# Kernel optimization log

Hardware: AMD Instinct MI355X
Metric: run time of the kernel (lower is better)

## Reference

```python
import jax, jax.numpy as jnp
import numpy as np

EPS = 1e-5

def lrelu(x):
    return jnp.where(x > 0, x, 0.2 * x)

def bn(x, g, b, ch_axis=1):
    # BatchNorm in training-mode math (batch statistics), affine
    axes = tuple(i for i in range(x.ndim) if i != ch_axis)
    m = x.mean(axes, keepdims=True)
    v = x.var(axes, keepdims=True)
    shp = [1] * x.ndim; shp[ch_axis] = -1
    return g.reshape(shp) * (x - m) / jnp.sqrt(v + EPS) + b.reshape(shp)

def get_graph_feature(x, idx):
    # x: (B,C,N), idx: (B,N,k) -> edge features (B,2C,N,k) = [neighbor - center, center]
    xt = jnp.transpose(x, (0, 2, 1))                      # (B,N,C)
    nb = jax.vmap(lambda pts, i: pts[i])(xt, idx)         # gather: (B,N,k,C)
    center = jnp.broadcast_to(xt[:, :, None, :], nb.shape)
    edge = jnp.concatenate([nb - center, center], axis=-1)  # (B,N,k,2C)
    return jnp.transpose(edge, (0, 3, 1, 2))              # (B,2C,N,k)

def setup_inputs() -> dict:
    key = jax.random.key(0)
    ks = jax.random.split(key, 12)
    B, N, K = 4, 2048, 20
    def w(k, o, c, s=0.05):
        return jax.random.normal(k, (o, c), jnp.float32) * s
    inp = {}
    inp["x"] = jax.random.normal(ks[0], (B, N, 3), jnp.float32)
    inp["start_neighs"] = jax.random.randint(ks[1], (B, N, K), 0, N)
    dims = [(6, 64), (128, 128), (256, 256), (512, 512)]
    for i, (ci, co) in enumerate(dims):
        inp["w%d" % i] = w(ks[2 + i], co, ci)
        inp["g%d" % i] = jnp.ones((co,), jnp.float32)
        inp["b%d" % i] = jnp.zeros((co,), jnp.float32)
    inp["w4"] = w(ks[6], 1024, 960)
    inp["g4"] = jnp.ones((1024,), jnp.float32); inp["b4"] = jnp.zeros((1024,), jnp.float32)
    inp["lw1"] = w(ks[7], 1024, 2048)
    inp["g6"] = jnp.ones((1024,), jnp.float32); inp["b6"] = jnp.zeros((1024,), jnp.float32)
    inp["lw2"] = w(ks[8], 512, 1024); inp["lb2"] = jnp.zeros((512,), jnp.float32)
    inp["g7"] = jnp.ones((512,), jnp.float32); inp["b7"] = jnp.zeros((512,), jnp.float32)
    inp["lw3"] = w(ks[9], 256, 512); inp["lb3"] = jnp.zeros((256,), jnp.float32)
    return inp

def reference(x, start_neighs,
              w0, g0, b0, w1, g1, b1, w2, g2, b2, w3, g3, b3,
              w4, g4, b4, lw1, g6, b6, lw2, lb2, g7, b7, lw3, lb3):
    # forward_per_point
    xt = jnp.transpose(x, (0, 2, 1))                      # (B,3,N)
    h = get_graph_feature(xt, start_neighs)               # (B,6,N,k)
    outs = []
    for (w, g, b) in ((w0, g0, b0), (w1, g1, b1), (w2, g2, b2), (w3, g3, b3)):
        if outs:  # only_true_neighs=True -> reuse start_neighs
            h = get_graph_feature(outs[-1], start_neighs)
        h = lrelu(bn(jnp.einsum('oc,bcnk->bonk', w, h), g, b))  # 1x1 Conv2d + BN + LeakyReLU
        outs.append(h.max(axis=-1))                       # max over k neighbors -> (B,C,N)
    cat = jnp.concatenate(outs, axis=1)                   # (B,960,N)
    feats = lrelu(bn(jnp.einsum('oc,bcn->bon', w4, cat), g4, b4))  # (B,1024,N)
    # aggregate_all_points (dropout p=0 -> identity)
    z = jnp.concatenate([feats.max(-1), feats.mean(-1)], axis=1)   # (B,2048)
    z = lrelu(bn(z @ lw1.T, g6, b6))
    z = lrelu(bn(z @ lw2.T + lb2, g7, b7))
    z = z @ lw3.T + lb3                                   # (B,256)
    # forward returns (aggregated.squeeze(-1), features_per_point.transpose(1,2)) = (z, (B,1024,N))
    return z, feats
```

## Files before the change

kernel.cpp:

```cpp
#include <hip/hip_runtime.h>
#include <cstddef>
#include <cstdint>

#define EPSBN 1e-5f
constexpr int B_ = 4, N_ = 2048, K_ = 20;

typedef __attribute__((ext_vector_type(8))) _Float16 half8v;
typedef __attribute__((ext_vector_type(4))) float f32x4;
typedef const __attribute__((address_space(1))) unsigned int* gas_t;
typedef __attribute__((address_space(3))) unsigned int* las_t;

__device__ __forceinline__ void swz_batch(int B, int& b, int& local) {
    b = (B & 7) >> 1;
    local = ((B >> 3) << 1) | (B & 1);
}


__device__ __forceinline__ void prep_conv(const float* __restrict__ W, _Float16* __restrict__ W2h,
                                          int O, int C, int i) {
    int o = i / C, c = i - o * C;
    float a = W[o * 2 * C + c];
    float d = W[o * 2 * C + C + c] - a;
    W2h[(size_t)o * C + c] = (_Float16)a;
    W2h[(size_t)(O + o) * C + c] = (_Float16)d;
}

__global__ void k_prep_all(const float* __restrict__ w1, const float* __restrict__ w2,
                           const float* __restrict__ w3, const float* __restrict__ w4,
                           _Float16* __restrict__ W2h1, _Float16* __restrict__ W2h2,
                           _Float16* __restrict__ W2h3, _Float16* __restrict__ w4h) {
    int i = blockIdx.x * 256 + threadIdx.x;
    if (i < 8192) { prep_conv(w1, W2h1, 128, 64, i); return; }
    i -= 8192;
    if (i < 32768) { prep_conv(w2, W2h2, 256, 128, i); return; }
    i -= 32768;
    if (i < 131072) { prep_conv(w3, W2h3, 512, 256, i); return; }
    i -= 131072;
    if (i < 983040) w4h[i] = (_Float16)w4[i];
}

template<bool STATS, int BM>
__global__ __launch_bounds__(256, 3)
void k_gemm(const _Float16* __restrict__ A, int sa,
            const _Float16* __restrict__ Bw, int K,
            _Float16* __restrict__ outp, int so,
            float* __restrict__ psum, float* __restrict__ psq) {
    constexpr int MI = BM / 32;
    __shared__ __align__(16) _Float16 Als[BM * 64];
    __shared__ __align__(16) _Float16 Bls[128 * 64];
    const int tid = threadIdx.x, lane = tid & 63, w = tid >> 6;
    int bsw, lsw;
    swz_batch(blockIdx.x, bsw, lsw);
    constexpr int TPB = 2048 / BM;
    const int m0 = (bsw * TPB + lsw) * BM;
    const int n0 = blockIdx.y * 128;
    const int wr = (w >> 1) * (BM / 2), wc = (w & 1) * 64;

    f32x4 acc[MI][4];
#pragma unroll
    for (int i = 0; i < MI; ++i)
#pragma unroll
        for (int j = 0; j < 4; ++j) acc[i][j] = (f32x4){0.f, 0.f, 0.f, 0.f};

    int srb[4], scb[4];
#pragma unroll
    for (int j = 0; j < 4; ++j) {
        int idx = w * 256 + j * 64 + lane;
        srb[j] = idx >> 3;
        scb[j] = ((idx & 7) ^ (srb[j] & 7)) * 8;
    }
    int sra[MI], sca[MI];
#pragma unroll
    for (int j = 0; j < MI; ++j) {
        int idx = w * (MI * 64) + j * 64 + lane;
        sra[j] = idx >> 3;
        sca[j] = ((idx & 7) ^ (sra[j] & 7)) * 8;
    }
    int aoff[MI][2], boff[4][2];
#pragma unroll
    for (int i = 0; i < MI; ++i) {
        int ra = wr + i * 16 + (lane & 15);
#pragma unroll
        for (int t = 0; t < 2; ++t)
            aoff[i][t] = ra * 64 + ((((lane >> 4) + t * 4) ^ (ra & 7)) * 8);
    }
#pragma unroll
    for (int j = 0; j < 4; ++j) {
        int rb = wc + j * 16 + (lane & 15);
#pragma unroll
        for (int t = 0; t < 2; ++t)
            boff[j][t] = rb * 64 + ((((lane >> 4) + t * 4) ^ (rb & 7)) * 8);
    }

    for (int c0 = 0; c0 < K; c0 += 64) {
#pragma unroll
        for (int j = 0; j < MI; ++j) {
            const _Float16* ga = &A[(size_t)(m0 + sra[j]) * sa + c0 + sca[j]];
            __builtin_amdgcn_global_load_lds((gas_t)(const void*)ga,
                                             (las_t)(void*)&Als[(w * MI * 64 + j * 64) * 8], 16, 0, 0);
        }
#pragma unroll
        for (int j = 0; j < 4; ++j) {
            const _Float16* gb = &Bw[(size_t)(n0 + srb[j]) * K + c0 + scb[j]];
            __builtin_amdgcn_global_load_lds((gas_t)(const void*)gb,
                                             (las_t)(void*)&Bls[(w * 256 + j * 64) * 8], 16, 0, 0);
        }
        __syncthreads();
#pragma unroll
        for (int t = 0; t < 2; ++t) {
            half8v a[MI], b[4];
#pragma unroll
            for (int i = 0; i < MI; ++i) a[i] = *(const half8v*)&Als[aoff[i][t]];
#pragma unroll
            for (int j = 0; j < 4; ++j) b[j] = *(const half8v*)&Bls[boff[j][t]];
#pragma unroll
            for (int i = 0; i < MI; ++i)
#pragma unroll
                for (int j = 0; j < 4; ++j)
                    acc[i][j] = __builtin_amdgcn_mfma_f32_16x16x32_f16(a[i], b[j], acc[i][j], 0, 0, 0);
        }
        __syncthreads();
    }
#pragma unroll
    for (int i = 0; i < MI; ++i)
#pragma unroll
        for (int j = 0; j < 4; ++j)
#pragma unroll
            for (int e = 0; e < 4; ++e) {
                int row = m0 + wr + i * 16 + (lane >> 4) * 4 + e;
                int col = n0 + wc + j * 16 + (lane & 15);
                outp[(size_t)row * so + col] = (_Float16)acc[i][j][e];
            }
    if constexpr (STATS) {
        int slice = blockIdx.x & 63;
#pragma unroll
        for (int j = 0; j < 4; ++j) {
            float s = 0.f, q = 0.f;
#pragma unroll
            for (int i = 0; i < MI; ++i)
#pragma unroll
                for (int e = 0; e < 4; ++e) {
                    float v = acc[i][j][e];
                    s += v; q += v * v;
                }
            s += __shfl_xor(s, 16); s += __shfl_xor(s, 32);
            q += __shfl_xor(q, 16); q += __shfl_xor(q, 32);
            if ((lane >> 4) == 0) {
                int col = n0 + wc + j * 16 + lane;
                atomicAdd(&psum[slice * 1024 + col], s);
                atomicAdd(&psq[slice * 1024 + col], q);
            }
        }
    }
}

__global__ __launch_bounds__(256)
void k_gather0(const float* __restrict__ x, const float* __restrict__ w0,
               const int* __restrict__ nidx, const float* __restrict__ g,
               _Float16* __restrict__ exth,
               float* __restrict__ psum, float* __restrict__ psq) {
    constexpr int O = 64, VPT = 8, P = 32;
    __shared__ float s_red[P * O];
    __shared__ float q_red[P * O];
    const int tid = threadIdx.x;
    const int pl = tid / VPT, v = tid % VPT;
    int bsw, local;
    swz_batch(blockIdx.x, bsw, local);
    const int bbase = bsw * N_;
    const int p = bbase + local * P + pl;
    float wa[8][3], wd[8][3], sg[8];
#pragma unroll
    for (int e = 0; e < 8; ++e) {
        int o = v * 8 + e;
        float a0 = w0[o * 6], a1 = w0[o * 6 + 1], a2 = w0[o * 6 + 2];
        wa[e][0] = a0; wa[e][1] = a1; wa[e][2] = a2;
        wd[e][0] = w0[o * 6 + 3] - a0;
        wd[e][1] = w0[o * 6 + 4] - a1;
        wd[e][2] = w0[o * 6 + 5] - a2;
        sg[e] = (g[o] >= 0.f) ? 1.f : -1.f;
    }
    float mx[8], sm[8], sq[8];
#pragma unroll
    for (int e = 0; e < 8; ++e) { mx[e] = -3.4e38f; sm[e] = 0.f; sq[e] = 0.f; }
    const int* np = nidx + p * K_;
#pragma unroll 4
    for (int k = 0; k < K_; ++k) {
        int j = bbase + np[k];
        float x0 = x[j * 3], x1 = x[j * 3 + 1], x2 = x[j * 3 + 2];
#pragma unroll
        for (int e = 0; e < 8; ++e) {
            float f = wa[e][0] * x0 + wa[e][1] * x1 + wa[e][2] * x2;
            mx[e] = fmaxf(mx[e], f * sg[e]);
            sm[e] += f;
            sq[e] += f * f;
        }
    }
    float xp0 = x[p * 3], xp1 = x[p * 3 + 1], xp2 = x[p * 3 + 2];
    const float Kf = (float)K_;
    half8v exo;
#pragma unroll
    for (int e = 0; e < 8; ++e) {
        float zf = wd[e][0] * xp0 + wd[e][1] * xp1 + wd[e][2] * xp2;
        exo[e] = (_Float16)(sg[e] * mx[e] + zf);
        s_red[pl * O + v * 8 + e] = sm[e] + Kf * zf;
        q_red[pl * O + v * 8 + e] = sq[e] + 2.f * zf * sm[e] + Kf * zf * zf;
    }
    *(half8v*)&exth[(size_t)p * O + v * 8] = exo;
    __syncthreads();
    int slice = blockIdx.x & 63;
    for (int ch = tid; ch < O; ch += 256) {
        float s = 0.f, q = 0.f;
#pragma unroll
        for (int pp = 0; pp < P; ++pp) { s += s_red[pp * O + ch]; q += q_red[pp * O + ch]; }
        atomicAdd(&psum[slice * 1024 + ch], s);
        atomicAdd(&psq[slice * 1024 + ch], q);
    }
}

template<int O>
__global__ __launch_bounds__(256)
void k_gather(const _Float16* __restrict__ Z, const int* __restrict__ nidx,
              const float* __restrict__ g,
              _Float16* __restrict__ exth,
              float* __restrict__ psum, float* __restrict__ psq) {
    constexpr int VPT = O / 8, P = 256 / VPT;
    __shared__ float s_red[P * O];
    __shared__ float q_red[P * O];
    const int tid = threadIdx.x;
    const int pl = tid / VPT, v = tid % VPT;
    int bsw, local;
    swz_batch(blockIdx.x, bsw, local);
    const int bbase = bsw * N_;
    const int p = bbase + local * P + pl;
    float sg[8];
#pragma unroll
    for (int e = 0; e < 8; ++e) sg[e] = (g[v * 8 + e] >= 0.f) ? 1.f : -1.f;
    float mx[8], sm[8], sq[8];
#pragma unroll
    for (int e = 0; e < 8; ++e) { mx[e] = -3.4e38f; sm[e] = 0.f; sq[e] = 0.f; }
    const int* np = nidx + p * K_;
#pragma unroll 4
    for (int k = 0; k < K_; ++k) {
        int j = np[k];
        half8v z = *(const half8v*)&Z[(size_t)(bbase + j) * (2 * O) + v * 8];
#pragma unroll
        for (int e = 0; e < 8; ++e) {
            float f = (float)z[e];
            mx[e] = fmaxf(mx[e], f * sg[e]);
            sm[e] += f;
            sq[e] += f * f;
        }
    }
    half8v zd = *(const half8v*)&Z[(size_t)p * (2 * O) + O + v * 8];
    const float Kf = (float)K_;
    half8v exo;
#pragma unroll
    for (int e = 0; e < 8; ++e) {
        float zf = (float)zd[e];
        exo[e] = (_Float16)(sg[e] * mx[e] + zf);
        s_red[pl * O + v * 8 + e] = sm[e] + Kf * zf;
        q_red[pl * O + v * 8 + e] = sq[e] + 2.f * zf * sm[e] + Kf * zf * zf;
    }
    *(half8v*)&exth[(size_t)p * O + v * 8] = exo;
    __syncthreads();
    int slice = blockIdx.x & 63;
    for (int ch = tid; ch < O; ch += 256) {
        float s = 0.f, q = 0.f;
#pragma unroll
        for (int pp = 0; pp < P; ++pp) { s += s_red[pp * O + ch]; q += q_red[pp * O + ch]; }
        atomicAdd(&psum[slice * 1024 + ch], s);
        atomicAdd(&psq[slice * 1024 + ch], q);
    }
}

__global__ void k_finalize_sl(const float* __restrict__ psum, const float* __restrict__ psq,
                              const float* __restrict__ g, const float* __restrict__ b,
                              float cntInv, int O,
                              float* __restrict__ scale, float* __restrict__ shift) {
    int o = blockIdx.x * 256 + threadIdx.x;
    if (o >= O) return;
    float s = 0.f, q = 0.f;
    for (int i = 0; i < 64; ++i) { s += psum[i * 1024 + o]; q += psq[i * 1024 + o]; }
    float m = s * cntInv;
    float v = q * cntInv - m * m;
    float sc = g[o] * rsqrtf(fmaxf(v, 0.f) + EPSBN);
    scale[o] = sc;
    shift[o] = b[o] - m * sc;
}

template<int O>
__global__ void k_bn_apply(const _Float16* __restrict__ exth,
                           const float* __restrict__ scale, const float* __restrict__ shift,
                           _Float16* __restrict__ cath, int coff) {
    constexpr int PPB = 2048 / O;
    int bsw, local;
    swz_batch(blockIdx.x, bsw, local);
    const int pt_base = bsw * N_ + local * PPB;
    int tid = threadIdx.x;
    int pt = pt_base + (tid * 8) / O;
    int v8 = (tid * 8) & (O - 1);
    half8v hx = *(const half8v*)&exth[(size_t)pt * O + v8];
    half8v r;
#pragma unroll
    for (int e = 0; e < 8; ++e) {
        int o = v8 + e;
        float y = scale[o] * (float)hx[e] + shift[o];
        y = y > 0.f ? y : 0.2f * y;
        r[e] = (_Float16)y;
    }
    *(half8v*)&cath[(size_t)pt * 960 + coff + v8] = r;
}

__global__ void k_feats_out(const _Float16* __restrict__ Y4, const float* __restrict__ scale,
                            const float* __restrict__ shift, float* __restrict__ fo,
                            float* __restrict__ pmax, float* __restrict__ psumn) {
    __shared__ float tile[32][33];
    int tx = threadIdx.x, ty = threadIdx.y;
    int b = blockIdx.z;
    int n0 = blockIdx.x * 32, c0 = blockIdx.y * 32;
#pragma unroll
    for (int i = 0; i < 4; ++i) {
        int n = n0 + ty + i * 8;
        int c = c0 + tx;
        float v = (float)Y4[((size_t)(b * N_ + n)) * 1024 + c];
        v = scale[c] * v + shift[c];
        v = v > 0.f ? v : 0.2f * v;
        tile[ty + i * 8][tx] = v;
    }
    __syncthreads();
#pragma unroll
    for (int i = 0; i < 4; ++i) {
        int c = c0 + ty + i * 8;
        int n = n0 + tx;
        float v2 = tile[tx][ty + i * 8];
        fo[((size_t)(b * 1024 + c)) * N_ + n] = v2;
        float mx = v2, s = v2;
#pragma unroll
        for (int d = 1; d < 32; d <<= 1) {
            mx = fmaxf(mx, __shfl_xor(mx, d));
            s += __shfl_xor(s, d);
        }
        if (tx == 0) {
            int bc = (b << 10) + c;
            pmax[(size_t)bc * 64 + blockIdx.x] = mx;
            psumn[(size_t)bc * 64 + blockIdx.x] = s;
        }
    }
}

__global__ void k_pool2(const float* __restrict__ pmax, const float* __restrict__ psumn,
                        float* __restrict__ z0) {
    int bc = blockIdx.x * 4 + (threadIdx.x >> 6);
    int lane = threadIdx.x & 63;
    float mx = pmax[(size_t)bc * 64 + lane];
    float s  = psumn[(size_t)bc * 64 + lane];
#pragma unroll
    for (int d = 1; d < 64; d <<= 1) {
        mx = fmaxf(mx, __shfl_xor(mx, d));
        s += __shfl_xor(s, d);
    }
    if (lane == 0) {
        int b = bc >> 10, c = bc & 1023;
        z0[b * 2048 + c] = mx;
        z0[b * 2048 + 1024 + c] = s * (1.f / N_);
    }
}

__global__ void k_fc(const float* __restrict__ zin, const float* __restrict__ W,
                     const float* __restrict__ bias,
                     const float* __restrict__ gg, const float* __restrict__ gb,
                     int C, int O, float* __restrict__ zout) {
    __shared__ float sh4[4];
    const int b = threadIdx.x >> 6;
    const int lane = threadIdx.x & 63;
    const int o = blockIdx.x;
    const float* wr = W + (size_t)o * C;
    const float* zr = zin + b * C;
    float s = 0.f;
    for (int c = lane * 4; c < C; c += 256) {
        const float4 wv = *(const float4*)&wr[c];
        const float4 zv = *(const float4*)&zr[c];
        s += wv.x * zv.x + wv.y * zv.y + wv.z * zv.z + wv.w * zv.w;
    }
    s += __shfl_xor(s, 1);
    s += __shfl_xor(s, 2);
    s += __shfl_xor(s, 4);
    s += __shfl_xor(s, 8);
    s += __shfl_xor(s, 16);
    s += __shfl_xor(s, 32);
    if (!gg) {
        if (lane == 0) zout[b * O + o] = s + (bias ? bias[o] : 0.f);
        return;
    }
    if (lane == 0) sh4[b] = s + (bias ? bias[o] : 0.f);
    __syncthreads();
    if (threadIdx.x == 0) {
        float v0 = sh4[0], v1 = sh4[1], v2 = sh4[2], v3 = sh4[3];
        float m = 0.25f * (v0 + v1 + v2 + v3);
        float d0 = v0 - m, d1 = v1 - m, d2 = v2 - m, d3 = v3 - m;
        float var = 0.25f * (d0 * d0 + d1 * d1 + d2 * d2 + d3 * d3);
        float sc = gg[o] * rsqrtf(var + EPSBN);
        float shv = gb[o];
        float r0 = sc * d0 + shv, r1 = sc * d1 + shv, r2 = sc * d2 + shv, r3 = sc * d3 + shv;
        zout[o]         = r0 > 0.f ? r0 : 0.2f * r0;
        zout[O + o]     = r1 > 0.f ? r1 : 0.2f * r1;
        zout[2 * O + o] = r2 > 0.f ? r2 : 0.2f * r2;
        zout[3 * O + o] = r3 > 0.f ? r3 : 0.2f * r3;
    }
}


extern "C" void kernel_launch(void* const* d_in, const int* in_sizes, int n_in,
                              void* d_out, int out_size, void* d_ws, size_t ws_size,
                              hipStream_t stream) {
    const float* x    = (const float*)d_in[0];
    const int*   nidx = (const int*)d_in[1];
    const float* w[5]  = {(const float*)d_in[2], (const float*)d_in[5], (const float*)d_in[8],
                          (const float*)d_in[11], (const float*)d_in[14]};
    const float* g[5]  = {(const float*)d_in[3], (const float*)d_in[6], (const float*)d_in[9],
                          (const float*)d_in[12], (const float*)d_in[15]};
    const float* bb[5] = {(const float*)d_in[4], (const float*)d_in[7], (const float*)d_in[10],
                          (const float*)d_in[13], (const float*)d_in[16]};
    const float* lw1 = (const float*)d_in[17];
    const float* g6  = (const float*)d_in[18];
    const float* b6  = (const float*)d_in[19];
    const float* lw2 = (const float*)d_in[20];
    const float* lb2 = (const float*)d_in[21];
    const float* g7  = (const float*)d_in[22];
    const float* b7  = (const float*)d_in[23];
    const float* lw3 = (const float*)d_in[24];
    const float* lb3 = (const float*)d_in[25];

    float* out = (float*)d_out;
    float* fo  = out + 1024;

    uint8_t* base8 = (uint8_t*)d_ws;
    size_t off = 0;
    auto alloc = [&](size_t bytes) -> void* {
        void* r = base8 + off;
        off += (bytes + 255) & ~(size_t)255;
        return r;
    };
    _Float16* cath = (_Float16*)alloc((size_t)B_ * N_ * 960 * 2);
    _Float16* Z    = (_Float16*)alloc((size_t)8192 * 1024 * 2);
    _Float16* exth = (_Float16*)alloc((size_t)8192 * 512 * 2);
    _Float16* Y4   = (_Float16*)alloc((size_t)8192 * 1024 * 2);
    _Float16* W2h1 = (_Float16*)alloc((size_t)256 * 64 * 2);
    _Float16* W2h2 = (_Float16*)alloc((size_t)512 * 128 * 2);
    _Float16* W2h3 = (_Float16*)alloc((size_t)1024 * 256 * 2);
    _Float16* w4h  = (_Float16*)alloc((size_t)1024 * 960 * 2);
    float* psumall = (float*)alloc((size_t)5 * 131072 * 4);
    float* pmax  = (float*)alloc((size_t)4096 * 64 * 4);
    float* psumn = (float*)alloc((size_t)4096 * 64 * 4);
    float* scalev= (float*)alloc(1024 * 4);
    float* shiftv= (float*)alloc(1024 * 4);
    float* z0    = (float*)alloc(8192 * 4);
    float* z1    = (float*)alloc(4096 * 4);
    float* z2    = (float*)alloc(2048 * 4);
    (void)ws_size; (void)in_sizes; (void)n_in; (void)out_size;

    auto psumR = [&](int r) { return psumall + (size_t)r * 131072; };
    auto psqR  = [&](int r) { return psumall + (size_t)r * 131072 + 65536; };

    hipMemsetAsync(psumall, 0, (size_t)5 * 131072 * 4, stream);
    k_prep_all<<<(8192 + 32768 + 131072 + 983040 + 255) / 256, 256, 0, stream>>>(
        w[1], w[2], w[3], w[4], W2h1, W2h2, W2h3, w4h);

    k_gather0<<<256, 256, 0, stream>>>(x, w[0], nidx, g[0], exth, psumR(0), psqR(0));
    k_finalize_sl<<<1, 256, 0, stream>>>(psumR(0), psqR(0), g[0], bb[0], 1.f / (B_ * N_ * K_),
                                         64, scalev, shiftv);
    k_bn_apply<64><<<256, 256, 0, stream>>>(exth, scalev, shiftv, cath, 0);

    k_gemm<false, 64><<<dim3(128, 2), 256, 0, stream>>>(cath + 0, 960, W2h1, 64,
                                                        Z, 256, nullptr, nullptr);
    k_gather<128><<<512, 256, 0, stream>>>(Z, nidx, g[1], exth, psumR(1), psqR(1));
    k_finalize_sl<<<1, 256, 0, stream>>>(psumR(1), psqR(1), g[1], bb[1],
                                         1.f / (B_ * N_ * K_), 128, scalev, shiftv);
    k_bn_apply<128><<<512, 256, 0, stream>>>(exth, scalev, shiftv, cath, 64);

    k_gemm<false, 128><<<dim3(64, 4), 256, 0, stream>>>(cath + 64, 960, W2h2, 128,
                                                        Z, 512, nullptr, nullptr);
    k_gather<256><<<1024, 256, 0, stream>>>(Z, nidx, g[2], exth, psumR(2), psqR(2));
    k_finalize_sl<<<1, 256, 0, stream>>>(psumR(2), psqR(2), g[2], bb[2],
                                         1.f / (B_ * N_ * K_), 256, scalev, shiftv);
    k_bn_apply<256><<<1024, 256, 0, stream>>>(exth, scalev, shiftv, cath, 192);

    k_gemm<false, 128><<<dim3(64, 8), 256, 0, stream>>>(cath + 192, 960, W2h3, 256,
                                                        Z, 1024, nullptr, nullptr);
    k_gather<512><<<2048, 256, 0, stream>>>(Z, nidx, g[3], exth, psumR(3), psqR(3));
    k_finalize_sl<<<2, 256, 0, stream>>>(psumR(3), psqR(3), g[3], bb[3],
                                         1.f / (B_ * N_ * K_), 512, scalev, shiftv);
    k_bn_apply<512><<<2048, 256, 0, stream>>>(exth, scalev, shiftv, cath, 448);

    k_gemm<true, 128><<<dim3(64, 8), 256, 0, stream>>>(cath, 960, w4h, 960, Y4, 1024,
                                                       psumR(4), psqR(4));
    k_finalize_sl<<<4, 256, 0, stream>>>(psumR(4), psqR(4), g[4], bb[4], 1.f / (B_ * N_), 1024,
                                         scalev, shiftv);
    k_feats_out<<<dim3(64, 32, 4), dim3(32, 8), 0, stream>>>(Y4, scalev, shiftv, fo, pmax, psumn);
    k_pool2<<<1024, 256, 0, stream>>>(pmax, psumn, z0);

    k_fc<<<1024, 256, 0, stream>>>(z0, lw1, nullptr, g6, b6, 2048, 1024, z1);
    k_fc<<<512, 256, 0, stream>>>(z1, lw2, lb2, g7, b7, 1024, 512, z2);
    k_fc<<<256, 256, 0, stream>>>(z2, lw3, lb3, nullptr, nullptr, 512, 256, out);
}
```

Baseline: 168.9 us.

## Fuse BN finalize into apply kernels and pool via atomics into FC input

Replaces each per-layer finalize+apply kernel pair with one kernel that reduces the per-slice sums for its 64-channel tile and then applies BN+LeakyReLU. The global max/mean pooling kernel is removed: the feats kernel does an atomic max on an order-preserving uint key and an atomic add on the sum into z0, which is zeroed by an extended memset. The first FC decodes the keys and scales the mean. This cuts five kernel launches, but each BN block now redundantly rereads the 64-slice partial sums, and the pooling adds atomic contention.

```diff
diff --git a/kernel.cpp b/kernel.cpp
--- a/kernel.cpp
+++ b/kernel.cpp
@@ -13,6 +13,15 @@
 __device__ __forceinline__ void swz_batch(int B, int& b, int& local) {
     b = (B & 7) >> 1;
     local = ((B >> 3) << 1) | (B & 1);
+}
+
+__device__ __forceinline__ unsigned fkey(float x) {
+    unsigned u = __float_as_uint(x);
+    return (u & 0x80000000u) ? ~u : (u | 0x80000000u);
+}
+__device__ __forceinline__ float funkey(unsigned k) {
+    unsigned u = (k & 0x80000000u) ? (k ^ 0x80000000u) : ~k;
+    return __uint_as_float(u);
 }
 
 
@@ -273,6 +282,62 @@
     }
 }
 
+template<int O>
+__global__ __launch_bounds__(256)
+void k_bnfin(const _Float16* __restrict__ exth,
+             const float* __restrict__ psum, const float* __restrict__ psq,
+             const float* __restrict__ g, const float* __restrict__ b, float cntInv,
+             _Float16* __restrict__ cath, int coff) {
+    constexpr int NCT = O / 64;
+    __shared__ float part_s[64][4];
+    __shared__ float part_q[64][4];
+    __shared__ float scale_s[64], shift_s[64];
+    const int tid = threadIdx.x;
+    const int ct = blockIdx.x % NCT;
+    const int ptile = blockIdx.x / NCT;
+    int bsw, local;
+    swz_batch(ptile, bsw, local);
+    const int ch0 = ct * 64;
+    {
+        int lc = tid >> 2, q = tid & 3;
+        int ch = ch0 + lc;
+        float s = 0.f, qq = 0.f;
+        for (int i = q * 16; i < q * 16 + 16; ++i) {
+            s += psum[i * 1024 + ch];
+            qq += psq[i * 1024 + ch];
+        }
+        part_s[lc][q] = s; part_q[lc][q] = qq;
+    }
+    __syncthreads();
+    if ((tid & 3) == 0) {
+        int lc = tid >> 2;
+        float s = part_s[lc][0] + part_s[lc][1] + part_s[lc][2] + part_s[lc][3];
+        float qq = part_q[lc][0] + part_q[lc][1] + part_q[lc][2] + part_q[lc][3];
+        float m = s * cntInv;
+        float v = qq * cntInv - m * m;
+        float sc = g[ch0 + lc] * rsqrtf(fmaxf(v, 0.f) + EPSBN);
+        scale_s[lc] = sc;
+        shift_s[lc] = b[ch0 + lc] - m * sc;
+    }
+    __syncthreads();
+    const int pbase = bsw * N_ + local * 128;
+#pragma unroll
+    for (int r = 0; r < 4; ++r) {
+        int idx = r * 256 + tid;
+        int ptl = idx >> 3;
+        int cb = (idx & 7) * 8;
+        int p = pbase + ptl;
+        half8v hx = *(const half8v*)&exth[(size_t)p * O + ch0 + cb];
+        half8v rr;
+#pragma unroll
+        for (int e = 0; e < 8; ++e) {
+            float y = scale_s[cb + e] * (float)hx[e] + shift_s[cb + e];
+            rr[e] = (_Float16)(y > 0.f ? y : 0.2f * y);
+        }
+        *(half8v*)&cath[(size_t)p * 960 + coff + ch0 + cb] = rr;
+    }
+}
+
 __global__ void k_finalize_sl(const float* __restrict__ psum, const float* __restrict__ psq,
                               const float* __restrict__ g, const float* __restrict__ b,
                               float cntInv, int O,
@@ -288,32 +353,9 @@
     shift[o] = b[o] - m * sc;
 }
 
-template<int O>
-__global__ void k_bn_apply(const _Float16* __restrict__ exth,
-                           const float* __restrict__ scale, const float* __restrict__ shift,
-                           _Float16* __restrict__ cath, int coff) {
-    constexpr int PPB = 2048 / O;
-    int bsw, local;
-    swz_batch(blockIdx.x, bsw, local);
-    const int pt_base = bsw * N_ + local * PPB;
-    int tid = threadIdx.x;
-    int pt = pt_base + (tid * 8) / O;
-    int v8 = (tid * 8) & (O - 1);
-    half8v hx = *(const half8v*)&exth[(size_t)pt * O + v8];
-    half8v r;
-#pragma unroll
-    for (int e = 0; e < 8; ++e) {
-        int o = v8 + e;
-        float y = scale[o] * (float)hx[e] + shift[o];
-        y = y > 0.f ? y : 0.2f * y;
-        r[e] = (_Float16)y;
-    }
-    *(half8v*)&cath[(size_t)pt * 960 + coff + v8] = r;
-}
-
 __global__ void k_feats_out(const _Float16* __restrict__ Y4, const float* __restrict__ scale,
                             const float* __restrict__ shift, float* __restrict__ fo,
-                            float* __restrict__ pmax, float* __restrict__ psumn) {
+                            float* __restrict__ z0) {
     __shared__ float tile[32][33];
     int tx = threadIdx.x, ty = threadIdx.y;
     int b = blockIdx.z;
@@ -341,35 +383,16 @@
             s += __shfl_xor(s, d);
         }
         if (tx == 0) {
-            int bc = (b << 10) + c;
-            pmax[(size_t)bc * 64 + blockIdx.x] = mx;
-            psumn[(size_t)bc * 64 + blockIdx.x] = s;
-        }
-    }
-}
-
-__global__ void k_pool2(const float* __restrict__ pmax, const float* __restrict__ psumn,
-                        float* __restrict__ z0) {
-    int bc = blockIdx.x * 4 + (threadIdx.x >> 6);
-    int lane = threadIdx.x & 63;
-    float mx = pmax[(size_t)bc * 64 + lane];
-    float s  = psumn[(size_t)bc * 64 + lane];
-#pragma unroll
-    for (int d = 1; d < 64; d <<= 1) {
-        mx = fmaxf(mx, __shfl_xor(mx, d));
-        s += __shfl_xor(s, d);
-    }
-    if (lane == 0) {
-        int b = bc >> 10, c = bc & 1023;
-        z0[b * 2048 + c] = mx;
-        z0[b * 2048 + 1024 + c] = s * (1.f / N_);
+            atomicMax((unsigned*)&z0[b * 2048 + c], fkey(mx));
+            atomicAdd(&z0[b * 2048 + 1024 + c], s);
+        }
     }
 }
 
 __global__ void k_fc(const float* __restrict__ zin, const float* __restrict__ W,
                      const float* __restrict__ bias,
                      const float* __restrict__ gg, const float* __restrict__ gb,
-                     int C, int O, float* __restrict__ zout) {
+                     int C, int O, int pool, float* __restrict__ zout) {
     __shared__ float sh4[4];
     const int b = threadIdx.x >> 6;
     const int lane = threadIdx.x & 63;
@@ -379,7 +402,18 @@
     float s = 0.f;
     for (int c = lane * 4; c < C; c += 256) {
         const float4 wv = *(const float4*)&wr[c];
-        const float4 zv = *(const float4*)&zr[c];
+        float4 zv = *(const float4*)&zr[c];
+        if (pool) {
+            if (c < 1024) {
+                zv.x = funkey(__float_as_uint(zv.x));
+                zv.y = funkey(__float_as_uint(zv.y));
+                zv.z = funkey(__float_as_uint(zv.z));
+                zv.w = funkey(__float_as_uint(zv.w));
+            } else {
+                const float inv = 1.f / N_;
+                zv.x *= inv; zv.y *= inv; zv.z *= inv; zv.w *= inv;
+            }
+        }
         s += wv.x * zv.x + wv.y * zv.y + wv.z * zv.z + wv.w * zv.w;
     }
     s += __shfl_xor(s, 1);
@@ -450,11 +484,9 @@
     _Float16* W2h3 = (_Float16*)alloc((size_t)1024 * 256 * 2);
     _Float16* w4h  = (_Float16*)alloc((size_t)1024 * 960 * 2);
     float* psumall = (float*)alloc((size_t)5 * 131072 * 4);
-    float* pmax  = (float*)alloc((size_t)4096 * 64 * 4);
-    float* psumn = (float*)alloc((size_t)4096 * 64 * 4);
-    float* scalev= (float*)alloc(1024 * 4);
-    float* shiftv= (float*)alloc(1024 * 4);
-    float* z0    = (float*)alloc(8192 * 4);
+    float* z0      = (float*)alloc(8192 * 4);
+    float* scalev  = (float*)alloc(1024 * 4);
+    float* shiftv  = (float*)alloc(1024 * 4);
     float* z1    = (float*)alloc(4096 * 4);
     float* z2    = (float*)alloc(2048 * 4);
     (void)ws_size; (void)in_sizes; (void)n_in; (void)out_size;
@@ -462,44 +494,37 @@
     auto psumR = [&](int r) { return psumall + (size_t)r * 131072; };
     auto psqR  = [&](int r) { return psumall + (size_t)r * 131072 + 65536; };
 
-    hipMemsetAsync(psumall, 0, (size_t)5 * 131072 * 4, stream);
+    hipMemsetAsync(psumall, 0, (size_t)5 * 131072 * 4 + 8192 * 4, stream);
     k_prep_all<<<(8192 + 32768 + 131072 + 983040 + 255) / 256, 256, 0, stream>>>(
         w[1], w[2], w[3], w[4], W2h1, W2h2, W2h3, w4h);
 
+    const float invK = 1.f / (B_ * N_ * K_);
+
     k_gather0<<<256, 256, 0, stream>>>(x, w[0], nidx, g[0], exth, psumR(0), psqR(0));
-    k_finalize_sl<<<1, 256, 0, stream>>>(psumR(0), psqR(0), g[0], bb[0], 1.f / (B_ * N_ * K_),
-                                         64, scalev, shiftv);
-    k_bn_apply<64><<<256, 256, 0, stream>>>(exth, scalev, shiftv, cath, 0);
+    k_bnfin<64><<<64, 256, 0, stream>>>(exth, psumR(0), psqR(0), g[0], bb[0], invK, cath, 0);
 
     k_gemm<false, 64><<<dim3(128, 2), 256, 0, stream>>>(cath + 0, 960, W2h1, 64,
                                                         Z, 256, nullptr, nullptr);
     k_gather<128><<<512, 256, 0, stream>>>(Z, nidx, g[1], exth, psumR(1), psqR(1));
-    k_finalize_sl<<<1, 256, 0, stream>>>(psumR(1), psqR(1), g[1], bb[1],
-                                         1.f / (B_ * N_ * K_), 128, scalev, shiftv);
-    k_bn_apply<128><<<512, 256, 0, stream>>>(exth, scalev, shiftv, cath, 64);
+    k_bnfin<128><<<128, 256, 0, stream>>>(exth, psumR(1), psqR(1), g[1], bb[1], invK, cath, 64);
 
     k_gemm<false, 128><<<dim3(64, 4), 256, 0, stream>>>(cath + 64, 960, W2h2, 128,
                                                         Z, 512, nullptr, nullptr);
     k_gather<256><<<1024, 256, 0, stream>>>(Z, nidx, g[2], exth, psumR(2), psqR(2));
-    k_finalize_sl<<<1, 256, 0, stream>>>(psumR(2), psqR(2), g[2], bb[2],
-                                         1.f / (B_ * N_ * K_), 256, scalev, shiftv);
-    k_bn_apply<256><<<1024, 256, 0, stream>>>(exth, scalev, shiftv, cath, 192);
+    k_bnfin<256><<<256, 256, 0, stream>>>(exth, psumR(2), psqR(2), g[2], bb[2], invK, cath, 192);
 
     k_gemm<false, 128><<<dim3(64, 8), 256, 0, stream>>>(cath + 192, 960, W2h3, 256,
                                                         Z, 1024, nullptr, nullptr);
     k_gather<512><<<2048, 256, 0, stream>>>(Z, nidx, g[3], exth, psumR(3), psqR(3));
-    k_finalize_sl<<<2, 256, 0, stream>>>(psumR(3), psqR(3), g[3], bb[3],
-                                         1.f / (B_ * N_ * K_), 512, scalev, shiftv);
-    k_bn_apply<512><<<2048, 256, 0, stream>>>(exth, scalev, shiftv, cath, 448);
+    k_bnfin<512><<<512, 256, 0, stream>>>(exth, psumR(3), psqR(3), g[3], bb[3], invK, cath, 448);
 
     k_gemm<true, 128><<<dim3(64, 8), 256, 0, stream>>>(cath, 960, w4h, 960, Y4, 1024,
                                                        psumR(4), psqR(4));
     k_finalize_sl<<<4, 256, 0, stream>>>(psumR(4), psqR(4), g[4], bb[4], 1.f / (B_ * N_), 1024,
                                          scalev, shiftv);
-    k_feats_out<<<dim3(64, 32, 4), dim3(32, 8), 0, stream>>>(Y4, scalev, shiftv, fo, pmax, psumn);
-    k_pool2<<<1024, 256, 0, stream>>>(pmax, psumn, z0);
-
-    k_fc<<<1024, 256, 0, stream>>>(z0, lw1, nullptr, g6, b6, 2048, 1024, z1);
-    k_fc<<<512, 256, 0, stream>>>(z1, lw2, lb2, g7, b7, 1024, 512, z2);
-    k_fc<<<256, 256, 0, stream>>>(z2, lw3, lb3, nullptr, nullptr, 512, 256, out);
-}
+    k_feats_out<<<dim3(64, 32, 4), dim3(32, 8), 0, stream>>>(Y4, scalev, shiftv, fo, z0);
+
+    k_fc<<<1024, 256, 0, stream>>>(z0, lw1, nullptr, g6, b6, 2048, 1024, 1, z1);
+    k_fc<<<512, 256, 0, stream>>>(z1, lw2, lb2, g7, b7, 1024, 512, 0, z2);
+    k_fc<<<256, 256, 0, stream>>>(z2, lw3, lb3, nullptr, nullptr, 512, 256, 0, out);
+}
```

New measurement: 176.2 us. 4.3% more time.
